# Kernel optimization log

Measured on AMD Instinct MI355X. Metric: run time of the kernel, lower is better.

## Reference

```python
import jax, jax.numpy as jnp
import numpy as np

B, N, E, C = 4, 4096, 128, 64

def setup_inputs() -> dict:
    key = jax.random.key(0)
    ks = jax.random.split(key, 12)
    s = 1.0 / np.sqrt(E)
    sc = 1.0 / np.sqrt(C)
    return {
        "X": jax.random.normal(ks[0], (B, N, E), jnp.float32),
        "context": jax.random.normal(ks[1], (B, C), jnp.float32),
        "Wq": jax.random.uniform(ks[2], (E, E), jnp.float32, -s, s),
        "bq": jax.random.uniform(ks[3], (E,), jnp.float32, -s, s),
        "Wk": jax.random.uniform(ks[4], (E, E), jnp.float32, -s, s),
        "bk": jax.random.uniform(ks[5], (E,), jnp.float32, -s, s),
        "Wv": jax.random.uniform(ks[6], (E, E), jnp.float32, -s, s),
        "bv": jax.random.uniform(ks[7], (E,), jnp.float32, -s, s),
        "Wc": jax.random.uniform(ks[8], (E, C), jnp.float32, -sc, sc),
        "bc": jax.random.uniform(ks[9], (E,), jnp.float32, -sc, sc),
    }

def reference(X, context, Wq, bq, Wk, bk, Wv, bv, Wc, bc):
    scale = jnp.asarray(E ** 0.5, X.dtype)
    Q = jnp.einsum('bne,fe->bnf', X, Wq) + bq          # [B,N,E]
    K = jnp.einsum('bne,fe->bnf', X, Wk) + bk
    V = jnp.einsum('bne,fe->bnf', X, Wv) + bv
    scores = jnp.einsum('bne,bme->bnm', Q, K) / scale  # [B,N,N]
    ctx = (jnp.einsum('bc,ec->be', context, Wc) + bc)  # [B,E] context bias
    # Q @ ctx^T -> [B,N,1], broadcast-added across key dim
    bias = jnp.einsum('bne,be->bn', Q, ctx)[:, :, None]
    w = jax.nn.softmax(scores + bias, axis=-1)
    return jnp.einsum('bnm,bme->bne', w, V)
```

## Files before the change

### kernel.cpp

```cpp
#include <hip/hip_runtime.h>
#include <hip/hip_bf16.h>

typedef short short8 __attribute__((ext_vector_type(8)));
typedef float f32x4 __attribute__((ext_vector_type(4)));
typedef float f32x16 __attribute__((ext_vector_type(16)));
typedef int int4v __attribute__((ext_vector_type(4)));
typedef unsigned short ushort4v __attribute__((ext_vector_type(4)));

#define NB 4
#define NS 4096
#define NE 128
#define ALPHA 0.1275174468f
#define KVB 64
#define NIT (NS / KVB)
#define SPLITS 4
#define DEFER_THR 8.0f

static __device__ __forceinline__ unsigned short f2bf(float f) {
  union { float f; unsigned int u; } v; v.f = f;
  unsigned int u = v.u;
  return (unsigned short)((u + 0x7FFFu + ((u >> 16) & 1u)) >> 16);
}
static __device__ __forceinline__ unsigned int pack2bf(float a, float b) {
  union { __hip_bfloat162 h; unsigned int u; } v;
  v.h = __float22bfloat162_rn(float2{a, b});
  return v.u;
}
static __device__ __forceinline__ short8 as_s8(int4v x) {
  union { int4v i; short8 s; } u; u.i = x; return u.s;
}


__global__ __launch_bounds__(256) void prep_k(
    const float* __restrict__ Wq, const float* __restrict__ Wk,
    const float* __restrict__ Wv,
    unsigned short* __restrict__ Wqb, unsigned short* __restrict__ Wkb,
    unsigned short* __restrict__ Wvb) {
  int i = blockIdx.x * 256 + threadIdx.x;
  const float* srcs[3] = {Wq, Wk, Wv};
  unsigned short* dsts[3] = {Wqb, Wkb, Wvb};
  int m = i >> 12, off = (i & 4095) * 4;
  float4 v = *(const float4*)(srcs[m] + off);
  ushort4v o;
  o[0] = f2bf(v.x); o[1] = f2bf(v.y); o[2] = f2bf(v.z); o[3] = f2bf(v.w);
  *(ushort4v*)(dsts[m] + off) = o;
}

static __device__ __forceinline__ f32x4 wtile(const short8 xa[4],
                                              const unsigned short* __restrict__ Wb,
                                              int fb, int g, int li) {
  f32x4 acc = {0.f, 0.f, 0.f, 0.f};
  #pragma unroll
  for (int ks = 0; ks < 4; ++ks) {
    short8 wf = *(const short8*)(Wb + (fb * 16 + li) * NE + ks * 32 + g * 8);
    acc = __builtin_amdgcn_mfma_f32_16x16x32_bf16(xa[ks], wf, acc, 0, 0, 0);
  }
  return acc;
}

__global__ __launch_bounds__(256) void qkv_proj_k(
    const float* __restrict__ X,
    const unsigned short* __restrict__ Wqb, const float* __restrict__ bq,
    const unsigned short* __restrict__ Wkb, const float* __restrict__ bk,
    const unsigned short* __restrict__ Wvb, const float* __restrict__ bv,
    unsigned short* __restrict__ Qs, unsigned short* __restrict__ Kd,
    unsigned short* __restrict__ VT) {
  const int lane = threadIdx.x & 63;
  const int wv   = threadIdx.x >> 6;
  const int tile = (blockIdx.x >> 1) * 4 + wv;
  const int fb0  = (blockIdx.x & 1) * 4;
  const int m0   = tile * 16;
  const int g    = lane >> 4, li = lane & 15;

  short8 xa[4];
  #pragma unroll
  for (int ks = 0; ks < 4; ++ks) {
    const float* xp = X + (size_t)(m0 + li) * NE + ks * 32 + g * 8;
    float4 x0 = *(const float4*)xp;
    float4 x1 = *(const float4*)(xp + 4);
    short8 t;
    t[0] = (short)f2bf(x0.x); t[1] = (short)f2bf(x0.y);
    t[2] = (short)f2bf(x0.z); t[3] = (short)f2bf(x0.w);
    t[4] = (short)f2bf(x1.x); t[5] = (short)f2bf(x1.y);
    t[6] = (short)f2bf(x1.z); t[7] = (short)f2bf(x1.w);
    xa[ks] = t;
  }

  const int bb  = m0 >> 12;
  const int tT  = (m0 & 4095) >> 6;
  const int jtT = (m0 >> 4) & 3;
  const size_t tgbase = ((size_t)(bb * 64 + tT)) * 16;

  #pragma unroll
  for (int f2 = 0; f2 < 4; ++f2) {
    const int fb = fb0 + f2;
    f32x4 aq = wtile(xa, Wqb, fb, g, li);
    float biq = bq[fb * 16 + li];
    #pragma unroll
    for (int r = 0; r < 4; ++r)
      Qs[(size_t)(m0 + g * 4 + r) * NE + fb * 16 + li] = f2bf((aq[r] + biq) * ALPHA);
    f32x4 ak = wtile(xa, Wkb, fb, g, li);
    float bik = bk[fb * 16 + li];
    unsigned short* kdst = Kd + (tgbase + jtT * 4 + (fb >> 1)) * 512 +
                           ((fb & 1) * 2 + (li >> 3)) * 128 + (li & 7);
    #pragma unroll
    for (int r = 0; r < 4; ++r)
      kdst[(g * 4 + r) * 8] = f2bf(ak[r] + bik);
    f32x4 av = wtile(xa, Wvb, fb, g, li);
    float biv = bv[fb * 16 + li];
    ushort4v pv;
    #pragma unroll
    for (int r = 0; r < 4; ++r) pv[r] = f2bf(av[r] + biv);
    *(ushort4v*)(VT + (tgbase + jtT * 4 + (fb >> 1)) * 512 +
                 ((g >> 1) * 32 + (fb & 1) * 16 + li) * 8 + (g & 1) * 4) = pv;
  }
}

__global__ __launch_bounds__(512, 2) void attn_k(
    const unsigned short* __restrict__ Qs, const unsigned short* __restrict__ Kd,
    const unsigned short* __restrict__ VT, float* __restrict__ Out) {
  __shared__ float smO[2 * SPLITS * 4 * 64 * 16];
  __shared__ float smML[2 * SPLITS * 64];

  const int lane = threadIdx.x & 63;
  const int wv   = threadIdx.x >> 6;
  const int qg   = wv >> 2;
  const int sp   = wv & 3;
  const int bi   = blockIdx.x;
  const int b    = (bi >> 1) & 3;
  const int within = ((bi >> 3) << 1) | (bi & 1);
  const int qb   = within * 64 + qg * 32;
  const int g    = lane >> 4, li = lane & 15;
  const int l31  = lane & 31, hi = lane >> 5;
  const bool qsel = (lane >> 4) & 1;

  int4v q00, q01, q02, q03, q10, q11, q12, q13;
  {
    const unsigned short* q0 = Qs + (size_t)(b * NS + qb + li) * NE + g * 8;
    const unsigned short* q1 = Qs + (size_t)(b * NS + qb + 16 + li) * NE + g * 8;
    unsigned long long a0 = (unsigned long long)q0, a1 = (unsigned long long)q1;
    asm volatile("global_load_dwordx4 %0, %1, off"             : "=v"(q00) : "v"(a0));
    asm volatile("global_load_dwordx4 %0, %1, off offset:64"   : "=v"(q01) : "v"(a0));
    asm volatile("global_load_dwordx4 %0, %1, off offset:128"  : "=v"(q02) : "v"(a0));
    asm volatile("global_load_dwordx4 %0, %1, off offset:192"  : "=v"(q03) : "v"(a0));
    asm volatile("global_load_dwordx4 %0, %1, off"             : "=v"(q10) : "v"(a1));
    asm volatile("global_load_dwordx4 %0, %1, off offset:64"   : "=v"(q11) : "v"(a1));
    asm volatile("global_load_dwordx4 %0, %1, off offset:128"  : "=v"(q12) : "v"(a1));
    asm volatile("global_load_dwordx4 %0, %1, off offset:192"  : "=v"(q13) : "v"(a1));
  }

  const size_t stbase = (size_t)b * 64 * 16 * 512;
  const int    kvoff  = sp * 2048 + lane * 8;
  const unsigned long long kbase =
      (unsigned long long)(Kd + stbase + kvoff);
  const unsigned long long vbase =
      (unsigned long long)(VT + stbase + kvoff);

  int4v ka0, ka1, ka2, ka3, va0, va1, va2, va3;
  int4v kb0, kb1, kb2, kb3, vb0, vb1, vb2, vb3;

  #define LOAD_SET(K0,K1,K2,K3,V0,V1,V2,V3,T)                                   \
    {                                                                           \
      unsigned long long ka_ = kbase + (unsigned long long)(T) * 16384;         \
      unsigned long long va_ = vbase + (unsigned long long)(T) * 16384;         \
      asm volatile("global_load_dwordx4 %0, %1, off"             : "=v"(K0) : "v"(ka_)); \
      asm volatile("global_load_dwordx4 %0, %1, off offset:1024" : "=v"(K1) : "v"(ka_)); \
      asm volatile("global_load_dwordx4 %0, %1, off offset:2048" : "=v"(K2) : "v"(ka_)); \
      asm volatile("global_load_dwordx4 %0, %1, off offset:3072" : "=v"(K3) : "v"(ka_)); \
      asm volatile("global_load_dwordx4 %0, %1, off"             : "=v"(V0) : "v"(va_)); \
      asm volatile("global_load_dwordx4 %0, %1, off offset:1024" : "=v"(V1) : "v"(va_)); \
      asm volatile("global_load_dwordx4 %0, %1, off offset:2048" : "=v"(V2) : "v"(va_)); \
      asm volatile("global_load_dwordx4 %0, %1, off offset:3072" : "=v"(V3) : "v"(va_)); \
    }
  #define LOAD_A(T) LOAD_SET(ka0,ka1,ka2,ka3,va0,va1,va2,va3,T)
  #define LOAD_B(T) LOAD_SET(kb0,kb1,kb2,kb3,vb0,vb1,vb2,vb3,T)
  #define WAIT8 asm volatile("s_waitcnt vmcnt(8)" ::: "memory"); \
                __builtin_amdgcn_sched_barrier(0);

  f32x16 o[4];
  #pragma unroll
  for (int et = 0; et < 4; ++et)
    #pragma unroll
    for (int r = 0; r < 16; ++r) o[et][r] = 0.f;
  float m0 = -1e30f, m1 = -1e30f, L0 = 0.f, L1 = 0.f;

  const int src01 = (lane & 15) | (lane & 32);
  const int src23 = src01 + 16;

  #define BODY(K0,K1,K2,K3,V0,V1,V2,V3)                                        \
  {                                                                            \
    f32x4 s0 = {0.f, 0.f, 0.f, 0.f}, s1 = {0.f, 0.f, 0.f, 0.f};                \
    __builtin_amdgcn_s_setprio(1);                                             \
    s0 = __builtin_amdgcn_mfma_f32_16x16x32_bf16(as_s8(K0), as_s8(q00), s0, 0,0,0); \
    s1 = __builtin_amdgcn_mfma_f32_16x16x32_bf16(as_s8(K0), as_s8(q10), s1, 0,0,0); \
    s0 = __builtin_amdgcn_mfma_f32_16x16x32_bf16(as_s8(K1), as_s8(q01), s0, 0,0,0); \
    s1 = __builtin_amdgcn_mfma_f32_16x16x32_bf16(as_s8(K1), as_s8(q11), s1, 0,0,0); \
    s0 = __builtin_amdgcn_mfma_f32_16x16x32_bf16(as_s8(K2), as_s8(q02), s0, 0,0,0); \
    s1 = __builtin_amdgcn_mfma_f32_16x16x32_bf16(as_s8(K2), as_s8(q12), s1, 0,0,0); \
    s0 = __builtin_amdgcn_mfma_f32_16x16x32_bf16(as_s8(K3), as_s8(q03), s0, 0,0,0); \
    s1 = __builtin_amdgcn_mfma_f32_16x16x32_bf16(as_s8(K3), as_s8(q13), s1, 0,0,0); \
    __builtin_amdgcn_s_setprio(0);                                             \
    float tm0 = fmaxf(fmaxf(s0[0], s0[1]), fmaxf(s0[2], s0[3]));               \
    float tm1 = fmaxf(fmaxf(s1[0], s1[1]), fmaxf(s1[2], s1[3]));               \
    if (__any(fmaxf(tm0 - m0, tm1 - m1) > DEFER_THR)) {                        \
      tm0 = fmaxf(tm0, __shfl_xor(tm0, 16));                                   \
      tm1 = fmaxf(tm1, __shfl_xor(tm1, 16));                                   \
      tm0 = fmaxf(tm0, __shfl_xor(tm0, 32));                                   \
      tm1 = fmaxf(tm1, __shfl_xor(tm1, 32));                                   \
      float mn0 = fmaxf(m0, tm0), c0 = __builtin_amdgcn_exp2f(m0 - mn0);       \
      float mn1 = fmaxf(m1, tm1), c1 = __builtin_amdgcn_exp2f(m1 - mn1);       \
      const float cmy = qsel ? c1 : c0;                                        \
      o[0] = o[0] * cmy; o[1] = o[1] * cmy;                                    \
      o[2] = o[2] * cmy; o[3] = o[3] * cmy;                                    \
      L0 *= c0; L1 *= c1; m0 = mn0; m1 = mn1;                                  \
    }                                                                          \
    float p00 = __builtin_amdgcn_exp2f(s0[0] - m0);                            \
    float p01 = __builtin_amdgcn_exp2f(s0[1] - m0);                            \
    float p02 = __builtin_amdgcn_exp2f(s0[2] - m0);                            \
    float p03 = __builtin_amdgcn_exp2f(s0[3] - m0);                            \
    float p10 = __builtin_amdgcn_exp2f(s1[0] - m1);                            \
    float p11 = __builtin_amdgcn_exp2f(s1[1] - m1);                            \
    float p12 = __builtin_amdgcn_exp2f(s1[2] - m1);                            \
    float p13 = __builtin_amdgcn_exp2f(s1[3] - m1);                            \
    L0 += (p00 + p01) + (p02 + p03);                                           \
    L1 += (p10 + p11) + (p12 + p13);                                           \
    unsigned int pk00 = pack2bf(p00, p01);                                     \
    unsigned int pk01 = pack2bf(p02, p03);                                     \
    unsigned int pk10 = pack2bf(p10, p11);                                     \
    unsigned int pk11 = pack2bf(p12, p13);                                     \
    int ta, tb, w0, w1, w2, w3;                                                \
    ta = __shfl((int)pk00, src01); tb = __shfl((int)pk10, src01);              \
    w0 = qsel ? tb : ta;                                                       \
    ta = __shfl((int)pk01, src01); tb = __shfl((int)pk11, src01);              \
    w1 = qsel ? tb : ta;                                                       \
    ta = __shfl((int)pk00, src23); tb = __shfl((int)pk10, src23);              \
    w2 = qsel ? tb : ta;                                                       \
    ta = __shfl((int)pk01, src23); tb = __shfl((int)pk11, src23);              \
    w3 = qsel ? tb : ta;                                                       \
    union { int4v i4; short8 s8; } pb;                                         \
    pb.i4 = (int4v){w0, w1, w2, w3};                                           \
    __builtin_amdgcn_s_setprio(1);                                             \
    o[0] = __builtin_amdgcn_mfma_f32_32x32x16_bf16(as_s8(V0), pb.s8, o[0], 0,0,0); \
    o[1] = __builtin_amdgcn_mfma_f32_32x32x16_bf16(as_s8(V1), pb.s8, o[1], 0,0,0); \
    o[2] = __builtin_amdgcn_mfma_f32_32x32x16_bf16(as_s8(V2), pb.s8, o[2], 0,0,0); \
    o[3] = __builtin_amdgcn_mfma_f32_32x32x16_bf16(as_s8(V3), pb.s8, o[3], 0,0,0); \
    __builtin_amdgcn_s_setprio(0);                                             \
  }

  LOAD_A(0);
  WAIT8;

  #pragma unroll 1
  for (int t2 = 0; t2 < NIT; t2 += 2) {
    LOAD_B(t2 + 1);
    WAIT8;
    BODY(ka0, ka1, ka2, ka3, va0, va1, va2, va3)
    LOAD_A((t2 + 2) & (NIT - 1));
    WAIT8;
    BODY(kb0, kb1, kb2, kb3, vb0, vb1, vb2, vb3)
  }

  __syncthreads();

  L0 += __shfl_xor(L0, 16); L0 += __shfl_xor(L0, 32);
  L1 += __shfl_xor(L1, 16); L1 += __shfl_xor(L1, 32);
  #pragma unroll
  for (int et = 0; et < 4; ++et)
    #pragma unroll
    for (int rq = 0; rq < 4; ++rq) {
      float4 v;
      v.x = o[et][rq * 4 + 0]; v.y = o[et][rq * 4 + 1];
      v.z = o[et][rq * 4 + 2]; v.w = o[et][rq * 4 + 3];
      *(float4*)(smO + (size_t)(((qg * SPLITS + sp) * 4 + et) * 64 + lane) * 16 + rq * 4) = v;
    }
  if (lane < 16) {
    smML[(qg * SPLITS + sp) * 64 + lane]      = m0;
    smML[(qg * SPLITS + sp) * 64 + 16 + lane] = m1;
    smML[(qg * SPLITS + sp) * 64 + 32 + lane] = L0;
    smML[(qg * SPLITS + sp) * 64 + 48 + lane] = L1;
  }
  __syncthreads();

  const int cqg = wv >> 2, cet = wv & 3;
  float ms[SPLITS], Ls[SPLITS];
  #pragma unroll
  for (int sp2 = 0; sp2 < SPLITS; ++sp2) {
    ms[sp2] = smML[(cqg * SPLITS + sp2) * 64 + l31];
    Ls[sp2] = smML[(cqg * SPLITS + sp2) * 64 + 32 + l31];
  }
  float M = fmaxf(fmaxf(ms[0], ms[1]), fmaxf(ms[2], ms[3]));
  float W[SPLITS], Ltot = 0.f;
  #pragma unroll
  for (int sp2 = 0; sp2 < SPLITS; ++sp2) {
    W[sp2] = __builtin_amdgcn_exp2f(ms[sp2] - M);
    Ltot += W[sp2] * Ls[sp2];
  }
  const float rL = 1.f / Ltot;
  float* Orow = Out + (size_t)(b * NS + within * 64 + cqg * 32 + l31) * NE + cet * 32;
  #pragma unroll
  for (int rq = 0; rq < 4; ++rq) {
    float4 acc = make_float4(0.f, 0.f, 0.f, 0.f);
    #pragma unroll
    for (int sp2 = 0; sp2 < SPLITS; ++sp2) {
      float4 v = *(const float4*)(smO +
          (size_t)(((cqg * SPLITS + sp2) * 4 + cet) * 64 + lane) * 16 + rq * 4);
      acc.x += W[sp2] * v.x; acc.y += W[sp2] * v.y;
      acc.z += W[sp2] * v.z; acc.w += W[sp2] * v.w;
    }
    acc.x *= rL; acc.y *= rL; acc.z *= rL; acc.w *= rL;
    *(float4*)(Orow + 8 * rq + 4 * hi) = acc;
  }
}

extern "C" void kernel_launch(void* const* d_in, const int* in_sizes, int n_in,
                              void* d_out, int out_size, void* d_ws, size_t ws_size,
                              hipStream_t stream) {
  const float* X  = (const float*)d_in[0];
  const float* Wq = (const float*)d_in[2];
  const float* bq = (const float*)d_in[3];
  const float* Wk = (const float*)d_in[4];
  const float* bk = (const float*)d_in[5];
  const float* Wv = (const float*)d_in[6];
  const float* bv = (const float*)d_in[7];

  unsigned short* Qs  = (unsigned short*)d_ws;
  unsigned short* Kd  = Qs + (size_t)NB * NS * NE;
  unsigned short* VT  = Kd + (size_t)NB * NS * NE;
  unsigned short* Wqb = VT + (size_t)NB * NS * NE;
  unsigned short* Wkb = Wqb + NE * NE;
  unsigned short* Wvb = Wkb + NE * NE;

  prep_k<<<48, 256, 0, stream>>>(Wq, Wk, Wv, Wqb, Wkb, Wvb);
  qkv_proj_k<<<512, 256, 0, stream>>>(X, Wqb, bq, Wkb, bk, Wvb, bv, Qs, Kd, VT);
  attn_k<<<256, 512, 0, stream>>>(Qs, Kd, VT, (float*)d_out);
}
```

Measured before the change: 84.30 us.

## Pre-swizzle weights into MFMA fragment order and stage Q/K stores through LDS

The weight-prep kernel now writes bf16 weights in per-lane MFMA fragment order, so each lane in the projection kernel loads its B operand with one contiguous 16-byte read. The Q and K outputs, which were written as scattered 2-byte stores, are first gathered into per-wave shared-memory tiles and then written out with coalesced 16-byte stores. The aim is to cut uncoalesced global traffic in the projection kernel, at the cost of extra LDS use and an occupancy hint. The attention kernel, which likely dominates total time, is unchanged.

```diff
diff --git a/kernel.cpp b/kernel.cpp
--- a/kernel.cpp
+++ b/kernel.cpp
@@ -34,37 +34,46 @@
 __global__ __launch_bounds__(256) void prep_k(
     const float* __restrict__ Wq, const float* __restrict__ Wk,
     const float* __restrict__ Wv,
-    unsigned short* __restrict__ Wqb, unsigned short* __restrict__ Wkb,
-    unsigned short* __restrict__ Wvb) {
+    unsigned short* __restrict__ Wqf, unsigned short* __restrict__ Wkf,
+    unsigned short* __restrict__ Wvf) {
   int i = blockIdx.x * 256 + threadIdx.x;
   const float* srcs[3] = {Wq, Wk, Wv};
-  unsigned short* dsts[3] = {Wqb, Wkb, Wvb};
-  int m = i >> 12, off = (i & 4095) * 4;
-  float4 v = *(const float4*)(srcs[m] + off);
+  unsigned short* dsts[3] = {Wqf, Wkf, Wvf};
+  int m = i >> 12, j = i & 4095;
+  int group = j >> 7;
+  int l     = (j >> 1) & 63;
+  int e0    = (j & 1) * 4;
+  int fb = group >> 2, ks = group & 3;
+  int r  = fb * 16 + (l & 15);
+  int c  = ks * 32 + (l >> 4) * 8 + e0;
+  float4 v = *(const float4*)(srcs[m] + r * NE + c);
   ushort4v o;
   o[0] = f2bf(v.x); o[1] = f2bf(v.y); o[2] = f2bf(v.z); o[3] = f2bf(v.w);
-  *(ushort4v*)(dsts[m] + off) = o;
+  *(ushort4v*)(dsts[m] + (size_t)j * 4) = o;
 }
 
 static __device__ __forceinline__ f32x4 wtile(const short8 xa[4],
-                                              const unsigned short* __restrict__ Wb,
-                                              int fb, int g, int li) {
+                                              const unsigned short* __restrict__ Wf,
+                                              int fb, int lane) {
   f32x4 acc = {0.f, 0.f, 0.f, 0.f};
   #pragma unroll
   for (int ks = 0; ks < 4; ++ks) {
-    short8 wf = *(const short8*)(Wb + (fb * 16 + li) * NE + ks * 32 + g * 8);
+    short8 wf = *(const short8*)(Wf + ((fb * 4 + ks) << 9) + lane * 8);
     acc = __builtin_amdgcn_mfma_f32_16x16x32_bf16(xa[ks], wf, acc, 0, 0, 0);
   }
   return acc;
 }
 
-__global__ __launch_bounds__(256) void qkv_proj_k(
+__global__ __launch_bounds__(256, 4) void qkv_proj_k(
     const float* __restrict__ X,
-    const unsigned short* __restrict__ Wqb, const float* __restrict__ bq,
-    const unsigned short* __restrict__ Wkb, const float* __restrict__ bk,
-    const unsigned short* __restrict__ Wvb, const float* __restrict__ bv,
+    const unsigned short* __restrict__ Wqf, const float* __restrict__ bq,
+    const unsigned short* __restrict__ Wkf, const float* __restrict__ bk,
+    const unsigned short* __restrict__ Wvf, const float* __restrict__ bv,
     unsigned short* __restrict__ Qs, unsigned short* __restrict__ Kd,
     unsigned short* __restrict__ VT) {
+  __shared__ __align__(16) unsigned short qt[4][1024];
+  __shared__ __align__(16) unsigned short kt[4][1024];
+
   const int lane = threadIdx.x & 63;
   const int wv   = threadIdx.x >> 6;
   const int tile = (blockIdx.x >> 1) * 4 + wv;
@@ -94,25 +103,34 @@
   #pragma unroll
   for (int f2 = 0; f2 < 4; ++f2) {
     const int fb = fb0 + f2;
-    f32x4 aq = wtile(xa, Wqb, fb, g, li);
+    f32x4 aq = wtile(xa, Wqf, fb, lane);
     float biq = bq[fb * 16 + li];
     #pragma unroll
     for (int r = 0; r < 4; ++r)
-      Qs[(size_t)(m0 + g * 4 + r) * NE + fb * 16 + li] = f2bf((aq[r] + biq) * ALPHA);
-    f32x4 ak = wtile(xa, Wkb, fb, g, li);
+      qt[wv][(g * 4 + r) * 64 + f2 * 16 + li] = f2bf((aq[r] + biq) * ALPHA);
+    f32x4 ak = wtile(xa, Wkf, fb, lane);
     float bik = bk[fb * 16 + li];
-    unsigned short* kdst = Kd + (tgbase + jtT * 4 + (fb >> 1)) * 512 +
-                           ((fb & 1) * 2 + (li >> 3)) * 128 + (li & 7);
+    const int hk  = f2 >> 1;
+    const int ggk = (fb & 1) * 2 + (li >> 3);
     #pragma unroll
     for (int r = 0; r < 4; ++r)
-      kdst[(g * 4 + r) * 8] = f2bf(ak[r] + bik);
-    f32x4 av = wtile(xa, Wvb, fb, g, li);
+      kt[wv][hk * 512 + ggk * 128 + (g * 4 + r) * 8 + (li & 7)] = f2bf(ak[r] + bik);
+    f32x4 av = wtile(xa, Wvf, fb, lane);
     float biv = bv[fb * 16 + li];
     ushort4v pv;
     #pragma unroll
     for (int r = 0; r < 4; ++r) pv[r] = f2bf(av[r] + biv);
     *(ushort4v*)(VT + (tgbase + jtT * 4 + (fb >> 1)) * 512 +
                  ((g >> 1) * 32 + (fb & 1) * 16 + li) * 8 + (g & 1) * 4) = pv;
+  }
+
+  #pragma unroll
+  for (int r2 = 0; r2 < 2; ++r2) {
+    short8 qv = *(const short8*)&qt[wv][lane * 16 + r2 * 8];
+    *(short8*)(Qs + (size_t)(m0 + (lane >> 2)) * NE + fb0 * 16 +
+               (lane & 3) * 16 + r2 * 8) = qv;
+    short8 kv = *(const short8*)&kt[wv][r2 * 512 + lane * 8];
+    *(short8*)(Kd + (tgbase + jtT * 4 + (fb0 >> 1) + r2) * 512 + lane * 8) = kv;
   }
 }
 
@@ -326,11 +344,11 @@
   unsigned short* Qs  = (unsigned short*)d_ws;
   unsigned short* Kd  = Qs + (size_t)NB * NS * NE;
   unsigned short* VT  = Kd + (size_t)NB * NS * NE;
-  unsigned short* Wqb = VT + (size_t)NB * NS * NE;
-  unsigned short* Wkb = Wqb + NE * NE;
-  unsigned short* Wvb = Wkb + NE * NE;
-
-  prep_k<<<48, 256, 0, stream>>>(Wq, Wk, Wv, Wqb, Wkb, Wvb);
-  qkv_proj_k<<<512, 256, 0, stream>>>(X, Wqb, bq, Wkb, bk, Wvb, bv, Qs, Kd, VT);
+  unsigned short* Wqf = VT + (size_t)NB * NS * NE;
+  unsigned short* Wkf = Wqf + NE * NE;
+  unsigned short* Wvf = Wkf + NE * NE;
+
+  prep_k<<<48, 256, 0, stream>>>(Wq, Wk, Wv, Wqf, Wkf, Wvf);
+  qkv_proj_k<<<512, 256, 0, stream>>>(X, Wqf, bq, Wkf, bk, Wvf, bv, Qs, Kd, VT);
   attn_k<<<256, 512, 0, stream>>>(Qs, Kd, VT, (float*)d_out);
 }
```

After: 76.33 us, median of 2. 1.1x faster.
